# Kernel optimization log

Measured on AMD Instinct MI355X. Metric: run time of the kernel, lower is better.

Reference implementation:

```python
import jax, jax.numpy as jnp
import numpy as np

B, S, D_MODEL, H, D_HEAD = 1, 4096, 512, 8, 64
ROPE_BASE = 10000.0


def setup_inputs() -> dict:
    key = jax.random.key(0)
    ks = jax.random.split(key, 5)
    return {
        "hidden_states": jax.random.normal(ks[0], (B, S, D_MODEL), dtype=jnp.float32),
        "mask": jnp.zeros((B, H, S, S), dtype=jnp.float32),  # additive mask (0 = attend)
        "position_ids": jnp.broadcast_to(jnp.arange(S, dtype=jnp.int64), (B, S)),
        "Wq": jax.random.normal(ks[1], (D_MODEL, H * D_HEAD), dtype=jnp.float32) * 0.02,
        "Wk": jax.random.normal(ks[2], (D_MODEL, H * D_HEAD), dtype=jnp.float32) * 0.02,
        "Wv": jax.random.normal(ks[3], (D_MODEL, H * D_HEAD), dtype=jnp.float32) * 0.02,
        "Wo": jax.random.normal(ks[4], (H * D_HEAD, D_MODEL), dtype=jnp.float32) * 0.02,
    }


def _rope_cos_sin(position_ids, dtype):
    # inv_freq: [D_HEAD//2]
    inv_freq = 1.0 / (ROPE_BASE ** (jnp.arange(0, D_HEAD, 2, dtype=jnp.float32) / D_HEAD))
    freqs = position_ids.astype(jnp.float32)[:, :, None] * inv_freq[None, None, :]  # [b,s,d/2]
    emb = jnp.concatenate([freqs, freqs], axis=-1)  # [b,s,d]
    return jnp.cos(emb).astype(dtype), jnp.sin(emb).astype(dtype)


def _rotate_half(x):
    x1, x2 = x[..., : D_HEAD // 2], x[..., D_HEAD // 2 :]
    return jnp.concatenate([-x2, x1], axis=-1)


def reference(hidden_states, mask, position_ids, Wq, Wk, Wv, Wo):
    b, s, _ = hidden_states.shape
    shape = lambda x: x.reshape(b, s, H, D_HEAD).transpose(0, 2, 1, 3)  # b h s d
    q = shape(hidden_states @ Wq)
    k = shape(hidden_states @ Wk)
    v = shape(hidden_states @ Wv)

    cos, sin = _rope_cos_sin(position_ids, hidden_states.dtype)
    cos, sin = cos[:, None], sin[:, None]  # broadcast over heads
    q = q * cos + _rotate_half(q) * sin
    k = k * cos + _rotate_half(k) * sin

    # eager attention: NO 1/sqrt(d) scaling, matches the torch module
    scores = jnp.einsum("bhqd,bhkd->bhqk", q, k) + mask
    attn = jax.nn.softmax(scores.astype(jnp.float32), axis=-1).astype(scores.dtype)
    out = jnp.einsum("bhqk,bhkd->bhqd", attn, v)  # b h s d
    out = out.transpose(0, 2, 1, 3).reshape(b, s, H * D_HEAD)
    return out @ Wo
```

## Files before the change

### kernel.cpp

```cpp
#include <hip/hip_runtime.h>
#include <hip/hip_bf16.h>

typedef short s16x8 __attribute__((ext_vector_type(8)));
typedef float f32x4 __attribute__((ext_vector_type(4)));
typedef float f32x16 __attribute__((ext_vector_type(16)));

#define SQ 4096
#define DMODEL 512
#define NHEAD 8
#define DHEAD 64
#define LOG2E 1.4426950408889634f

static __device__ __forceinline__ unsigned short f2bf(float f) {
  unsigned int u = __float_as_uint(f);
  u += 0x7FFFu + ((u >> 16) & 1u);
  return (unsigned short)(u >> 16);
}

static __device__ __forceinline__ f32x4 MFMA16(s16x8 a, s16x8 b, f32x4 c) {
  return __builtin_amdgcn_mfma_f32_16x16x32_bf16(a, b, c, 0, 0, 0);
}
static __device__ __forceinline__ f32x16 MFMA32(s16x8 a, s16x8 b, f32x16 c) {
  return __builtin_amdgcn_mfma_f32_32x32x16_bf16(a, b, c, 0, 0, 0);
}
static __device__ __forceinline__ unsigned int cvtpk(float lo, float hi) {
  unsigned int r;
  asm("v_cvt_pk_bf16_f32 %0, %1, %2" : "=v"(r) : "v"(lo), "v"(hi));
  return r;
}
static __device__ __forceinline__ void plswap(unsigned int& x, unsigned int& y) {
  asm("v_permlane32_swap_b32 %0, %1" : "+v"(x), "+v"(y));
}
static __device__ __forceinline__ void gload_lds16(const unsigned short* g, unsigned short* l) {
  __builtin_amdgcn_global_load_lds((const __attribute__((address_space(1))) void*)g,
                                   (__attribute__((address_space(3))) void*)l, 16, 0, 0);
}

__global__ void rope_table_kernel(float* __restrict__ cos_t, float* __restrict__ sin_t) {
  int idx = blockIdx.x * 256 + threadIdx.x;
  int s = idx >> 5, i = idx & 31;
  float inv = exp2f(-(float)i * 0.4152410118609203f);
  float th = (float)s * inv;
  float sv, cv;
  sincosf(th, &sv, &cv);
  cos_t[idx] = cv;
  sin_t[idx] = sv;
}

__global__ __launch_bounds__(256) void qkv_kernel(
    const float* __restrict__ X, const float* __restrict__ Wq,
    const float* __restrict__ Wk, const float* __restrict__ Wv,
    const float* __restrict__ cos_t, const float* __restrict__ sin_t,
    unsigned short* __restrict__ Qf, unsigned short* __restrict__ Kf,
    unsigned short* __restrict__ Vf) {
  __shared__ __align__(16) unsigned short WT[64][40];
  __shared__ __align__(16) unsigned short Ts[64][72];
  const int pz = blockIdx.z;
  const float* __restrict__ W = (pz == 0) ? Wq : ((pz == 1) ? Wk : Wv);
  unsigned short* __restrict__ Out = (pz == 0) ? Qf : ((pz == 1) ? Kf : Vf);
  const int rb = blockIdx.x * 64;
  const int h  = blockIdx.y;
  const int cb = h * 64;
  const int t = threadIdx.x;
  const int w = t >> 6, l = t & 63;
  const int c = l & 15, g = l >> 4;

  f32x4 acc[4];
#pragma unroll
  for (int n = 0; n < 4; n++) acc[n] = (f32x4){0.f, 0.f, 0.f, 0.f};

  const int a2 = t >> 4;
  const int cm = (t & 15) * 4;
  const float* __restrict__ xp0 = X + (size_t)(rb + w * 16 + c) * DMODEL + g * 8;

  for (int kb = 0; kb < DMODEL; kb += 32) {
    {
      const float* wp = W + (size_t)(kb + 2 * a2) * DMODEL + cb + cm;
      float4 w0 = *(const float4*)wp;
      float4 w1 = *(const float4*)(wp + DMODEL);
      unsigned int p0 = (unsigned int)f2bf(w0.x) | ((unsigned int)f2bf(w1.x) << 16);
      unsigned int p1 = (unsigned int)f2bf(w0.y) | ((unsigned int)f2bf(w1.y) << 16);
      unsigned int p2 = (unsigned int)f2bf(w0.z) | ((unsigned int)f2bf(w1.z) << 16);
      unsigned int p3 = (unsigned int)f2bf(w0.w) | ((unsigned int)f2bf(w1.w) << 16);
      *(unsigned int*)&WT[cm + 0][2 * a2] = p0;
      *(unsigned int*)&WT[cm + 1][2 * a2] = p1;
      *(unsigned int*)&WT[cm + 2][2 * a2] = p2;
      *(unsigned int*)&WT[cm + 3][2 * a2] = p3;
    }
    __syncthreads();
    float4 x0 = *(const float4*)(xp0 + kb);
    float4 x1 = *(const float4*)(xp0 + kb + 4);
    s16x8 af;
    af[0] = (short)f2bf(x0.x); af[1] = (short)f2bf(x0.y);
    af[2] = (short)f2bf(x0.z); af[3] = (short)f2bf(x0.w);
    af[4] = (short)f2bf(x1.x); af[5] = (short)f2bf(x1.y);
    af[6] = (short)f2bf(x1.z); af[7] = (short)f2bf(x1.w);
#pragma unroll
    for (int n = 0; n < 4; n++) {
      s16x8 bf = *(const s16x8*)&WT[n * 16 + c][g * 8];
      acc[n] = MFMA16(af, bf, acc[n]);
    }
    __syncthreads();
  }

  if (pz < 2) {
    const float qs = (pz == 0) ? LOG2E : 1.0f;
#pragma unroll
    for (int n = 0; n < 2; n++)
#pragma unroll
      for (int i = 0; i < 4; i++) {
        int d = n * 16 + c;
        int sl = w * 16 + g * 4 + i;
        int s = rb + sl;
        float x1v = acc[n][i], x2v = acc[n + 2][i];
        float cv = cos_t[s * 32 + d];
        float sv = sin_t[s * 32 + d];
        Ts[sl][d]      = f2bf((x1v * cv - x2v * sv) * qs);
        Ts[sl][d + 32] = f2bf((x2v * cv + x1v * sv) * qs);
      }
    __syncthreads();
#pragma unroll
    for (int e = 0; e < 2; e++) {
      int f = t * 2 + e;
      int kg = f >> 8, m = (f >> 6) & 3, hif = (f >> 5) & 1, k32 = f & 31;
      s16x8 vv = *(const s16x8*)&Ts[kg * 32 + k32][m * 16 + hif * 8];
      size_t o16 = ((((size_t)h * 128 + (rb >> 5) + kg) * 4 + m) * 2 + hif) * 32 + k32;
      *(s16x8*)(Out + o16 * 8) = vv;
    }
  } else {
#pragma unroll
    for (int n = 0; n < 4; n++) {
      int d = n * 16 + c;
      int s0 = w * 16 + g * 4;
      unsigned int lo = (unsigned int)f2bf(acc[n][0]) | ((unsigned int)f2bf(acc[n][1]) << 16);
      unsigned int hi2 = (unsigned int)f2bf(acc[n][2]) | ((unsigned int)f2bf(acc[n][3]) << 16);
      *(unsigned int*)&Ts[d][s0]     = lo;
      *(unsigned int*)&Ts[d][s0 + 2] = hi2;
    }
    __syncthreads();
#pragma unroll
    for (int e = 0; e < 2; e++) {
      int f = t * 2 + e;
      int ktr = f >> 7, dc = (f >> 6) & 1, hif = (f >> 5) & 1, d32 = f & 31;
      s16x8 vv = *(const s16x8*)&Ts[dc * 32 + d32][ktr * 16 + hif * 8];
      size_t o16 = ((((size_t)h * 256 + (rb >> 4) + ktr) * 2 + dc) * 2 + hif) * 32 + d32;
      *(s16x8*)(Out + o16 * 8) = vv;
    }
  }
}

__global__ __launch_bounds__(256, 2) void attn_kernel(
    const unsigned short* __restrict__ Qf, const unsigned short* __restrict__ Kf,
    const unsigned short* __restrict__ Vf, float* __restrict__ Opart,
    float* __restrict__ Ml) {
  __shared__ __align__(16) unsigned short Sl[8192];
  const int h = blockIdx.y, part = blockIdx.z;
  const int qb = blockIdx.x * 128;
  const int t = threadIdx.x, w = t >> 6, l = t & 63;
  const int l31 = l & 31, hi = l >> 5;

  s16x8 qf[4];
  {
    const unsigned short* qp =
        Qf + ((((size_t)h * 128 + ((qb + w * 32) >> 5)) * 4) * 64 + l) * 8;
#pragma unroll
    for (int m = 0; m < 4; m++) qf[m] = *(const s16x8*)(qp + (size_t)m * 512);
  }
  f32x16 oacc0 = {}, oacc1 = {};
  float mi = -1e30f, li = 0.f;

  const unsigned short* Kit = Kf + ((size_t)h * 128 + part * 64) * 2048;
  const unsigned short* Vit = Vf + ((size_t)h * 256 + part * 128) * 1024;

  for (int it = 0; it < 32; ++it) {
    __syncthreads();
    {
      const unsigned short* src =
          (w < 2) ? (Kit + (size_t)it * 4096 + (size_t)w * 2048 + l * 8)
                  : (Vit + (size_t)it * 4096 + (size_t)(w - 2) * 2048 + l * 8);
      unsigned short* dst = Sl + w * 2048 + l * 8;
#pragma unroll
      for (int j = 0; j < 4; j++) gload_lds16(src + j * 512, dst + j * 512);
    }
    __syncthreads();

#pragma unroll
    for (int kgl = 0; kgl < 2; ++kgl) {
      s16x8 kf0 = *(const s16x8*)&Sl[kgl * 2048 + 0 * 512 + l * 8];
      s16x8 kf1 = *(const s16x8*)&Sl[kgl * 2048 + 1 * 512 + l * 8];
      s16x8 kf2 = *(const s16x8*)&Sl[kgl * 2048 + 2 * 512 + l * 8];
      s16x8 kf3 = *(const s16x8*)&Sl[kgl * 2048 + 3 * 512 + l * 8];
      f32x16 st = {};
      __builtin_amdgcn_s_setprio(1);
      st = MFMA32(kf0, qf[0], st);
      st = MFMA32(kf1, qf[1], st);
      st = MFMA32(kf2, qf[2], st);
      st = MFMA32(kf3, qf[3], st);
      __builtin_amdgcn_s_setprio(0);

      float tmax = st[0];
#pragma unroll
      for (int r = 1; r < 16; ++r) tmax = fmaxf(tmax, st[r]);
      tmax = fmaxf(tmax, __shfl_xor(tmax, 32));
      if (!__all(tmax <= mi + 8.0f)) {
        float mn = fmaxf(mi, tmax);
        float al = exp2f(mi - mn);
        mi = mn;
        li *= al;
#pragma unroll
        for (int r = 0; r < 16; ++r) {
          int qv = (r & 3) + 8 * (r >> 2) + 4 * hi;
          float aq = __shfl(al, qv);
          oacc0[r] *= aq;
          oacc1[r] *= aq;
        }
      }
      float p[16];
      float rs = 0.f;
#pragma unroll
      for (int r = 0; r < 16; ++r) {
        p[r] = exp2f(st[r] - mi);
        rs += p[r];
      }
      rs += __shfl_xor(rs, 32);
      li += rs;

      unsigned int u0 = cvtpk(p[0], p[1]),   u1 = cvtpk(p[2], p[3]);
      unsigned int u2 = cvtpk(p[4], p[5]),   u3 = cvtpk(p[6], p[7]);
      unsigned int u4 = cvtpk(p[8], p[9]),   u5 = cvtpk(p[10], p[11]);
      unsigned int u6 = cvtpk(p[12], p[13]), u7 = cvtpk(p[14], p[15]);
      plswap(u0, u2);
      plswap(u1, u3);
      plswap(u4, u6);
      plswap(u5, u7);
      union { unsigned int u[4]; s16x8 v; } P0, P1;
      P0.u[0] = u0; P0.u[1] = u1; P0.u[2] = u2; P0.u[3] = u3;
      P1.u[0] = u4; P1.u[1] = u5; P1.u[2] = u6; P1.u[3] = u7;

      s16x8 vf00 = *(const s16x8*)&Sl[4096 + (kgl * 2 + 0) * 1024 + 0 * 512 + l * 8];
      s16x8 vf01 = *(const s16x8*)&Sl[4096 + (kgl * 2 + 0) * 1024 + 1 * 512 + l * 8];
      s16x8 vf10 = *(const s16x8*)&Sl[4096 + (kgl * 2 + 1) * 1024 + 0 * 512 + l * 8];
      s16x8 vf11 = *(const s16x8*)&Sl[4096 + (kgl * 2 + 1) * 1024 + 1 * 512 + l * 8];
      __builtin_amdgcn_s_setprio(1);
      oacc0 = MFMA32(P0.v, vf00, oacc0);
      oacc1 = MFMA32(P0.v, vf01, oacc1);
      oacc0 = MFMA32(P1.v, vf10, oacc0);
      oacc1 = MFMA32(P1.v, vf11, oacc1);
      __builtin_amdgcn_s_setprio(0);
    }
  }

  float* Ob = Opart + (((size_t)(part * 8 + h) * 4096) + qb + w * 32) * 64;
#pragma unroll
  for (int r = 0; r < 16; ++r) {
    int qv = (r & 3) + 8 * (r >> 2) + 4 * hi;
    Ob[(size_t)qv * 64 + l31]      = oacc0[r];
    Ob[(size_t)qv * 64 + 32 + l31] = oacc1[r];
  }
  if (hi == 0) {
    float2 mlv = make_float2(mi, li);
    *(float2*)&Ml[((size_t)(part * 8 + h) * 4096 + qb + w * 32 + l31) * 2] = mlv;
  }
}

__global__ __launch_bounds__(256) void merge_kernel(
    const float* __restrict__ Opart, const float* __restrict__ Ml,
    unsigned short* __restrict__ AO) {
  int tid = blockIdx.x * 256 + threadIdx.x;
  int q = tid >> 9, hd = tid & 511, h = hd >> 6, d = hd & 63;
  size_t b1 = (size_t)h * 4096 + q;
  size_t b2 = (size_t)(8 + h) * 4096 + q;
  float m1 = Ml[b1 * 2], l1 = Ml[b1 * 2 + 1];
  float m2 = Ml[b2 * 2], l2 = Ml[b2 * 2 + 1];
  float mm = fmaxf(m1, m2);
  float w1 = exp2f(m1 - mm), w2 = exp2f(m2 - mm);
  float o = Opart[b1 * 64 + d] * w1 + Opart[b2 * 64 + d] * w2;
  AO[tid] = f2bf(o / (l1 * w1 + l2 * w2));
}

__global__ __launch_bounds__(256) void oproj_kernel(
    const unsigned short* __restrict__ A, const float* __restrict__ Wo,
    float* __restrict__ Out) {
  __shared__ __align__(16) unsigned short WT[64][40];
  const int rb = blockIdx.x * 64;
  const int cb = blockIdx.y * 64;
  const int t = threadIdx.x;
  const int w = t >> 6, l = t & 63;
  const int c = l & 15, g = l >> 4;

  f32x4 acc[4];
#pragma unroll
  for (int n = 0; n < 4; n++) acc[n] = (f32x4){0.f, 0.f, 0.f, 0.f};

  const int a2 = t >> 4, cm = (t & 15) * 4;
  const unsigned short* __restrict__ ap0 = A + (size_t)(rb + w * 16 + c) * DMODEL + g * 8;

  for (int kb = 0; kb < DMODEL; kb += 32) {
    {
      const float* wp = Wo + (size_t)(kb + 2 * a2) * DMODEL + cb + cm;
      float4 w0 = *(const float4*)wp;
      float4 w1 = *(const float4*)(wp + DMODEL);
      unsigned int p0 = (unsigned int)f2bf(w0.x) | ((unsigned int)f2bf(w1.x) << 16);
      unsigned int p1 = (unsigned int)f2bf(w0.y) | ((unsigned int)f2bf(w1.y) << 16);
      unsigned int p2 = (unsigned int)f2bf(w0.z) | ((unsigned int)f2bf(w1.z) << 16);
      unsigned int p3 = (unsigned int)f2bf(w0.w) | ((unsigned int)f2bf(w1.w) << 16);
      *(unsigned int*)&WT[cm + 0][2 * a2] = p0;
      *(unsigned int*)&WT[cm + 1][2 * a2] = p1;
      *(unsigned int*)&WT[cm + 2][2 * a2] = p2;
      *(unsigned int*)&WT[cm + 3][2 * a2] = p3;
    }
    __syncthreads();
    s16x8 af = *(const s16x8*)(ap0 + kb);
#pragma unroll
    for (int n = 0; n < 4; n++) {
      s16x8 bf = *(const s16x8*)&WT[n * 16 + c][g * 8];
      acc[n] = MFMA16(af, bf, acc[n]);
    }
    __syncthreads();
  }

#pragma unroll
  for (int n = 0; n < 4; n++)
#pragma unroll
    for (int i = 0; i < 4; i++) {
      int s = rb + w * 16 + g * 4 + i;
      Out[(size_t)s * DMODEL + cb + n * 16 + c] = acc[n][i];
    }
}

extern "C" void kernel_launch(void* const* d_in, const int* in_sizes, int n_in,
                              void* d_out, int out_size, void* d_ws, size_t ws_size,
                              hipStream_t stream) {
  const float* X  = (const float*)d_in[0];
  const float* Wq = (const float*)d_in[3];
  const float* Wk = (const float*)d_in[4];
  const float* Wv = (const float*)d_in[5];
  const float* Wo = (const float*)d_in[6];
  float* out = (float*)d_out;

  char* ws = (char*)d_ws;
  const size_t HSZ = (size_t)NHEAD * SQ * DHEAD;
  unsigned short* Qf = (unsigned short*)ws;
  unsigned short* Kf = Qf + HSZ;
  unsigned short* Vf = Kf + HSZ;
  unsigned short* AO = Vf + HSZ;
  float* Opart = (float*)(ws + 4 * HSZ * sizeof(unsigned short));
  float* Ml    = Opart + 2 * HSZ;
  float* cos_t = Ml + (size_t)2 * NHEAD * SQ * 2;
  float* sin_t = cos_t + (size_t)SQ * 32;

  rope_table_kernel<<<(SQ * 32) / 256, 256, 0, stream>>>(cos_t, sin_t);
  qkv_kernel<<<dim3(SQ / 64, NHEAD, 3), 256, 0, stream>>>(
      X, Wq, Wk, Wv, cos_t, sin_t, Qf, Kf, Vf);
  attn_kernel<<<dim3(SQ / 128, NHEAD, 2), 256, 0, stream>>>(Qf, Kf, Vf, Opart, Ml);
  merge_kernel<<<(int)(HSZ / 256), 256, 0, stream>>>(Opart, Ml, AO);
  oproj_kernel<<<dim3(SQ / 64, DMODEL / 64), 256, 0, stream>>>(AO, Wo, out);
}
```

Before: 132.9 us.

## Pre-convert weights to bf16, double-buffer LDS, fuse merge into oproj

A prep kernel now converts all four weight matrices to bf16 once, alongside building the RoPE table, so the GEMM kernels no longer convert fp32 weights in every tile. The qkv and oproj kernels double-buffer their weight tiles in LDS and prefetch the next k-slice into registers, which removes one barrier per iteration. The attention kernel double-buffers its K/V LDS stages so the next tile's global-to-LDS load overlaps compute. The split-KV merge is folded into oproj's A-operand load, removing a kernel launch and the AO round trip at the cost of more LDS and more registers.

```diff
diff --git a/kernel.cpp b/kernel.cpp
--- a/kernel.cpp
+++ b/kernel.cpp
@@ -1,6 +1,7 @@
 #include <hip/hip_runtime.h>
 #include <hip/hip_bf16.h>
 
+typedef short s16x4 __attribute__((ext_vector_type(4)));
 typedef short s16x8 __attribute__((ext_vector_type(8)));
 typedef float f32x4 __attribute__((ext_vector_type(4)));
 typedef float f32x16 __attribute__((ext_vector_type(16)));
@@ -36,27 +37,42 @@
                                    (__attribute__((address_space(3))) void*)l, 16, 0, 0);
 }
 
-__global__ void rope_table_kernel(float* __restrict__ cos_t, float* __restrict__ sin_t) {
-  int idx = blockIdx.x * 256 + threadIdx.x;
-  int s = idx >> 5, i = idx & 31;
-  float inv = exp2f(-(float)i * 0.4152410118609203f);
-  float th = (float)s * inv;
-  float sv, cv;
-  sincosf(th, &sv, &cv);
-  cos_t[idx] = cv;
-  sin_t[idx] = sv;
+__global__ void prep_kernel(const float* __restrict__ Wq, const float* __restrict__ Wk,
+                            const float* __restrict__ Wv, const float* __restrict__ Wo,
+                            float* __restrict__ cos_t, float* __restrict__ sin_t,
+                            unsigned short* __restrict__ WB) {
+  int b = blockIdx.x;
+  if (b < 512) {
+    int idx = b * 256 + threadIdx.x;
+    int s = idx >> 5, i = idx & 31;
+    float inv = exp2f(-(float)i * 0.4152410118609203f);
+    float th = (float)s * inv;
+    float sv, cv;
+    sincosf(th, &sv, &cv);
+    cos_t[idx] = cv;
+    sin_t[idx] = sv;
+  } else {
+    int bb = b - 512;
+    int mat = bb >> 8;
+    const float* __restrict__ W = (mat == 0) ? Wq : (mat == 1) ? Wk : (mat == 2) ? Wv : Wo;
+    int e = ((bb & 255) * 256 + threadIdx.x) * 4;
+    float4 v = *(const float4*)(W + e);
+    s16x4 o;
+    o[0] = (short)f2bf(v.x); o[1] = (short)f2bf(v.y);
+    o[2] = (short)f2bf(v.z); o[3] = (short)f2bf(v.w);
+    *(s16x4*)(WB + (size_t)mat * 262144 + e) = o;
+  }
 }
 
 __global__ __launch_bounds__(256) void qkv_kernel(
-    const float* __restrict__ X, const float* __restrict__ Wq,
-    const float* __restrict__ Wk, const float* __restrict__ Wv,
+    const float* __restrict__ X, const unsigned short* __restrict__ WB,
     const float* __restrict__ cos_t, const float* __restrict__ sin_t,
     unsigned short* __restrict__ Qf, unsigned short* __restrict__ Kf,
     unsigned short* __restrict__ Vf) {
-  __shared__ __align__(16) unsigned short WT[64][40];
+  __shared__ __align__(16) unsigned short WT[2][64][36];
   __shared__ __align__(16) unsigned short Ts[64][72];
   const int pz = blockIdx.z;
-  const float* __restrict__ W = (pz == 0) ? Wq : ((pz == 1) ? Wk : Wv);
+  const unsigned short* __restrict__ W = WB + (size_t)pz * 262144;
   unsigned short* __restrict__ Out = (pz == 0) ? Qf : ((pz == 1) ? Kf : Vf);
   const int rb = blockIdx.x * 64;
   const int h  = blockIdx.y;
@@ -65,40 +81,52 @@
   const int w = t >> 6, l = t & 63;
   const int c = l & 15, g = l >> 4;
 
-  f32x4 acc[4];
-#pragma unroll
-  for (int n = 0; n < 4; n++) acc[n] = (f32x4){0.f, 0.f, 0.f, 0.f};
-
+  f32x4 acc[4] = {};
   const int a2 = t >> 4;
   const int cm = (t & 15) * 4;
   const float* __restrict__ xp0 = X + (size_t)(rb + w * 16 + c) * DMODEL + g * 8;
-
-  for (int kb = 0; kb < DMODEL; kb += 32) {
-    {
-      const float* wp = W + (size_t)(kb + 2 * a2) * DMODEL + cb + cm;
-      float4 w0 = *(const float4*)wp;
-      float4 w1 = *(const float4*)(wp + DMODEL);
-      unsigned int p0 = (unsigned int)f2bf(w0.x) | ((unsigned int)f2bf(w1.x) << 16);
-      unsigned int p1 = (unsigned int)f2bf(w0.y) | ((unsigned int)f2bf(w1.y) << 16);
-      unsigned int p2 = (unsigned int)f2bf(w0.z) | ((unsigned int)f2bf(w1.z) << 16);
-      unsigned int p3 = (unsigned int)f2bf(w0.w) | ((unsigned int)f2bf(w1.w) << 16);
-      *(unsigned int*)&WT[cm + 0][2 * a2] = p0;
-      *(unsigned int*)&WT[cm + 1][2 * a2] = p1;
-      *(unsigned int*)&WT[cm + 2][2 * a2] = p2;
-      *(unsigned int*)&WT[cm + 3][2 * a2] = p3;
-    }
-    __syncthreads();
-    float4 x0 = *(const float4*)(xp0 + kb);
-    float4 x1 = *(const float4*)(xp0 + kb + 4);
+  const unsigned short* __restrict__ wp0 = W + (size_t)(2 * a2) * DMODEL + cb + cm;
+
+  {
+    s16x4 w0 = *(const s16x4*)wp0;
+    s16x4 w1 = *(const s16x4*)(wp0 + DMODEL);
+#pragma unroll
+    for (int j = 0; j < 4; j++)
+      *(unsigned int*)&WT[0][cm + j][2 * a2] =
+          (unsigned int)(unsigned short)w0[j] | ((unsigned int)(unsigned short)w1[j] << 16);
+  }
+  float4 xc0 = *(const float4*)xp0;
+  float4 xc1 = *(const float4*)(xp0 + 4);
+  __syncthreads();
+
+  for (int i = 0; i < 16; ++i) {
+    const int cur = i & 1;
+    s16x4 nw0, nw1;
+    float4 xn0, xn1;
+    if (i < 15) {
+      const unsigned short* wp = wp0 + (size_t)(i + 1) * 32 * DMODEL;
+      nw0 = *(const s16x4*)wp;
+      nw1 = *(const s16x4*)(wp + DMODEL);
+      xn0 = *(const float4*)(xp0 + (i + 1) * 32);
+      xn1 = *(const float4*)(xp0 + (i + 1) * 32 + 4);
+    }
     s16x8 af;
-    af[0] = (short)f2bf(x0.x); af[1] = (short)f2bf(x0.y);
-    af[2] = (short)f2bf(x0.z); af[3] = (short)f2bf(x0.w);
-    af[4] = (short)f2bf(x1.x); af[5] = (short)f2bf(x1.y);
-    af[6] = (short)f2bf(x1.z); af[7] = (short)f2bf(x1.w);
+    af[0] = (short)f2bf(xc0.x); af[1] = (short)f2bf(xc0.y);
+    af[2] = (short)f2bf(xc0.z); af[3] = (short)f2bf(xc0.w);
+    af[4] = (short)f2bf(xc1.x); af[5] = (short)f2bf(xc1.y);
+    af[6] = (short)f2bf(xc1.z); af[7] = (short)f2bf(xc1.w);
 #pragma unroll
     for (int n = 0; n < 4; n++) {
-      s16x8 bf = *(const s16x8*)&WT[n * 16 + c][g * 8];
+      s16x8 bf = *(const s16x8*)&WT[cur][n * 16 + c][g * 8];
       acc[n] = MFMA16(af, bf, acc[n]);
+    }
+    if (i < 15) {
+#pragma unroll
+      for (int j = 0; j < 4; j++)
+        *(unsigned int*)&WT[cur ^ 1][cm + j][2 * a2] =
+            (unsigned int)(unsigned short)nw0[j] | ((unsigned int)(unsigned short)nw1[j] << 16);
+      xc0 = xn0;
+      xc1 = xn1;
     }
     __syncthreads();
   }
@@ -153,7 +181,7 @@
     const unsigned short* __restrict__ Qf, const unsigned short* __restrict__ Kf,
     const unsigned short* __restrict__ Vf, float* __restrict__ Opart,
     float* __restrict__ Ml) {
-  __shared__ __align__(16) unsigned short Sl[8192];
+  __shared__ __align__(16) unsigned short Sl[2][8192];
   const int h = blockIdx.y, part = blockIdx.z;
   const int qb = blockIdx.x * 128;
   const int t = threadIdx.x, w = t >> 6, l = t & 63;
@@ -172,24 +200,34 @@
   const unsigned short* Kit = Kf + ((size_t)h * 128 + part * 64) * 2048;
   const unsigned short* Vit = Vf + ((size_t)h * 256 + part * 128) * 1024;
 
+#define STAGE(buf, it)                                                                  \
+  {                                                                                     \
+    const unsigned short* src =                                                         \
+        (w < 2) ? (Kit + (size_t)(it) * 4096 + (size_t)w * 2048 + l * 8)                \
+                : (Vit + (size_t)(it) * 4096 + (size_t)(w - 2) * 2048 + l * 8);         \
+    unsigned short* dst = &Sl[buf][w * 2048 + l * 8];                                   \
+    gload_lds16(src + 0 * 512, dst + 0 * 512);                                          \
+    gload_lds16(src + 1 * 512, dst + 1 * 512);                                          \
+    gload_lds16(src + 2 * 512, dst + 2 * 512);                                          \
+    gload_lds16(src + 3 * 512, dst + 3 * 512);                                          \
+  }
+
+  STAGE(0, 0);
+  asm volatile("s_waitcnt vmcnt(0)" ::: "memory");
+  __builtin_amdgcn_s_barrier();
+  asm volatile("" ::: "memory");
+
   for (int it = 0; it < 32; ++it) {
-    __syncthreads();
-    {
-      const unsigned short* src =
-          (w < 2) ? (Kit + (size_t)it * 4096 + (size_t)w * 2048 + l * 8)
-                  : (Vit + (size_t)it * 4096 + (size_t)(w - 2) * 2048 + l * 8);
-      unsigned short* dst = Sl + w * 2048 + l * 8;
-#pragma unroll
-      for (int j = 0; j < 4; j++) gload_lds16(src + j * 512, dst + j * 512);
-    }
-    __syncthreads();
+    const int cur = it & 1;
+    if (it < 31) STAGE(cur ^ 1, it + 1);
+    const unsigned short* Sb = &Sl[cur][0];
 
 #pragma unroll
     for (int kgl = 0; kgl < 2; ++kgl) {
-      s16x8 kf0 = *(const s16x8*)&Sl[kgl * 2048 + 0 * 512 + l * 8];
-      s16x8 kf1 = *(const s16x8*)&Sl[kgl * 2048 + 1 * 512 + l * 8];
-      s16x8 kf2 = *(const s16x8*)&Sl[kgl * 2048 + 2 * 512 + l * 8];
-      s16x8 kf3 = *(const s16x8*)&Sl[kgl * 2048 + 3 * 512 + l * 8];
+      s16x8 kf0 = *(const s16x8*)&Sb[kgl * 2048 + 0 * 512 + l * 8];
+      s16x8 kf1 = *(const s16x8*)&Sb[kgl * 2048 + 1 * 512 + l * 8];
+      s16x8 kf2 = *(const s16x8*)&Sb[kgl * 2048 + 2 * 512 + l * 8];
+      s16x8 kf3 = *(const s16x8*)&Sb[kgl * 2048 + 3 * 512 + l * 8];
       f32x16 st = {};
       __builtin_amdgcn_s_setprio(1);
       st = MFMA32(kf0, qf[0], st);
@@ -237,10 +275,10 @@
       P0.u[0] = u0; P0.u[1] = u1; P0.u[2] = u2; P0.u[3] = u3;
       P1.u[0] = u4; P1.u[1] = u5; P1.u[2] = u6; P1.u[3] = u7;
 
-      s16x8 vf00 = *(const s16x8*)&Sl[4096 + (kgl * 2 + 0) * 1024 + 0 * 512 + l * 8];
-      s16x8 vf01 = *(const s16x8*)&Sl[4096 + (kgl * 2 + 0) * 1024 + 1 * 512 + l * 8];
-      s16x8 vf10 = *(const s16x8*)&Sl[4096 + (kgl * 2 + 1) * 1024 + 0 * 512 + l * 8];
-      s16x8 vf11 = *(const s16x8*)&Sl[4096 + (kgl * 2 + 1) * 1024 + 1 * 512 + l * 8];
+      s16x8 vf00 = *(const s16x8*)&Sb[4096 + (kgl * 2 + 0) * 1024 + 0 * 512 + l * 8];
+      s16x8 vf01 = *(const s16x8*)&Sb[4096 + (kgl * 2 + 0) * 1024 + 1 * 512 + l * 8];
+      s16x8 vf10 = *(const s16x8*)&Sb[4096 + (kgl * 2 + 1) * 1024 + 0 * 512 + l * 8];
+      s16x8 vf11 = *(const s16x8*)&Sb[4096 + (kgl * 2 + 1) * 1024 + 1 * 512 + l * 8];
       __builtin_amdgcn_s_setprio(1);
       oacc0 = MFMA32(P0.v, vf00, oacc0);
       oacc1 = MFMA32(P0.v, vf01, oacc1);
@@ -248,7 +286,12 @@
       oacc1 = MFMA32(P1.v, vf11, oacc1);
       __builtin_amdgcn_s_setprio(0);
     }
-  }
+
+    asm volatile("s_waitcnt vmcnt(0)" ::: "memory");
+    __builtin_amdgcn_s_barrier();
+    asm volatile("" ::: "memory");
+  }
+#undef STAGE
 
   float* Ob = Opart + (((size_t)(part * 8 + h) * 4096) + qb + w * 32) * 64;
 #pragma unroll
@@ -263,68 +306,93 @@
   }
 }
 
-__global__ __launch_bounds__(256) void merge_kernel(
+__global__ __launch_bounds__(256) void oproj_kernel(
     const float* __restrict__ Opart, const float* __restrict__ Ml,
-    unsigned short* __restrict__ AO) {
-  int tid = blockIdx.x * 256 + threadIdx.x;
-  int q = tid >> 9, hd = tid & 511, h = hd >> 6, d = hd & 63;
-  size_t b1 = (size_t)h * 4096 + q;
-  size_t b2 = (size_t)(8 + h) * 4096 + q;
-  float m1 = Ml[b1 * 2], l1 = Ml[b1 * 2 + 1];
-  float m2 = Ml[b2 * 2], l2 = Ml[b2 * 2 + 1];
-  float mm = fmaxf(m1, m2);
-  float w1 = exp2f(m1 - mm), w2 = exp2f(m2 - mm);
-  float o = Opart[b1 * 64 + d] * w1 + Opart[b2 * 64 + d] * w2;
-  AO[tid] = f2bf(o / (l1 * w1 + l2 * w2));
-}
-
-__global__ __launch_bounds__(256) void oproj_kernel(
-    const unsigned short* __restrict__ A, const float* __restrict__ Wo,
-    float* __restrict__ Out) {
-  __shared__ __align__(16) unsigned short WT[64][40];
+    const unsigned short* __restrict__ WoB, float* __restrict__ Out) {
+  __shared__ __align__(16) unsigned short WT[2][64][36];
   const int rb = blockIdx.x * 64;
   const int cb = blockIdx.y * 64;
   const int t = threadIdx.x;
   const int w = t >> 6, l = t & 63;
   const int c = l & 15, g = l >> 4;
 
-  f32x4 acc[4];
-#pragma unroll
-  for (int n = 0; n < 4; n++) acc[n] = (f32x4){0.f, 0.f, 0.f, 0.f};
-
+  f32x4 acc[4] = {};
   const int a2 = t >> 4, cm = (t & 15) * 4;
-  const unsigned short* __restrict__ ap0 = A + (size_t)(rb + w * 16 + c) * DMODEL + g * 8;
-
-  for (int kb = 0; kb < DMODEL; kb += 32) {
-    {
-      const float* wp = Wo + (size_t)(kb + 2 * a2) * DMODEL + cb + cm;
-      float4 w0 = *(const float4*)wp;
-      float4 w1 = *(const float4*)(wp + DMODEL);
-      unsigned int p0 = (unsigned int)f2bf(w0.x) | ((unsigned int)f2bf(w1.x) << 16);
-      unsigned int p1 = (unsigned int)f2bf(w0.y) | ((unsigned int)f2bf(w1.y) << 16);
-      unsigned int p2 = (unsigned int)f2bf(w0.z) | ((unsigned int)f2bf(w1.z) << 16);
-      unsigned int p3 = (unsigned int)f2bf(w0.w) | ((unsigned int)f2bf(w1.w) << 16);
-      *(unsigned int*)&WT[cm + 0][2 * a2] = p0;
-      *(unsigned int*)&WT[cm + 1][2 * a2] = p1;
-      *(unsigned int*)&WT[cm + 2][2 * a2] = p2;
-      *(unsigned int*)&WT[cm + 3][2 * a2] = p3;
+  const int s = rb + w * 16 + c;
+
+  float a1[8], a2w[8];
+#pragma unroll
+  for (int hh = 0; hh < 8; hh++) {
+    float2 ml1 = *(const float2*)&Ml[((size_t)hh * 4096 + s) * 2];
+    float2 ml2 = *(const float2*)&Ml[((size_t)(8 + hh) * 4096 + s) * 2];
+    float mm = fmaxf(ml1.x, ml2.x);
+    float w1 = exp2f(ml1.x - mm), w2 = exp2f(ml2.x - mm);
+    float invL = 1.0f / (ml1.y * w1 + ml2.y * w2);
+    a1[hh] = w1 * invL;
+    a2w[hh] = w2 * invL;
+  }
+
+  const unsigned short* __restrict__ wp0 = WoB + (size_t)(2 * a2) * DMODEL + cb + cm;
+  {
+    s16x4 w0 = *(const s16x4*)wp0;
+    s16x4 w1 = *(const s16x4*)(wp0 + DMODEL);
+#pragma unroll
+    for (int j = 0; j < 4; j++)
+      *(unsigned int*)&WT[0][cm + j][2 * a2] =
+          (unsigned int)(unsigned short)w0[j] | ((unsigned int)(unsigned short)w1[j] << 16);
+  }
+  const float* op1b = Opart + (size_t)s * 64 + g * 8;
+  const float* op2b = op1b + (size_t)8 * 4096 * 64;
+  float4 pa0 = *(const float4*)op1b, pa1 = *(const float4*)(op1b + 4);
+  float4 pb0 = *(const float4*)op2b, pb1 = *(const float4*)(op2b + 4);
+  __syncthreads();
+
+#pragma unroll
+  for (int i = 0; i < 16; ++i) {
+    const int cur = i & 1;
+    const int hh = i >> 1;
+    s16x4 nw0, nw1;
+    float4 na0, na1, nb0, nb1;
+    if (i < 15) {
+      const unsigned short* wp = wp0 + (size_t)(i + 1) * 32 * DMODEL;
+      nw0 = *(const s16x4*)wp;
+      nw1 = *(const s16x4*)(wp + DMODEL);
+      size_t ao = (size_t)(i + 1 >> 1) * 4096 * 64 + ((i + 1) & 1) * 32;
+      na0 = *(const float4*)(op1b + ao);
+      na1 = *(const float4*)(op1b + ao + 4);
+      nb0 = *(const float4*)(op2b + ao);
+      nb1 = *(const float4*)(op2b + ao + 4);
+    }
+    s16x8 af;
+    af[0] = (short)f2bf(pa0.x * a1[hh] + pb0.x * a2w[hh]);
+    af[1] = (short)f2bf(pa0.y * a1[hh] + pb0.y * a2w[hh]);
+    af[2] = (short)f2bf(pa0.z * a1[hh] + pb0.z * a2w[hh]);
+    af[3] = (short)f2bf(pa0.w * a1[hh] + pb0.w * a2w[hh]);
+    af[4] = (short)f2bf(pa1.x * a1[hh] + pb1.x * a2w[hh]);
+    af[5] = (short)f2bf(pa1.y * a1[hh] + pb1.y * a2w[hh]);
+    af[6] = (short)f2bf(pa1.z * a1[hh] + pb1.z * a2w[hh]);
+    af[7] = (short)f2bf(pa1.w * a1[hh] + pb1.w * a2w[hh]);
+#pragma unroll
+    for (int n = 0; n < 4; n++) {
+      s16x8 bf = *(const s16x8*)&WT[cur][n * 16 + c][g * 8];
+      acc[n] = MFMA16(af, bf, acc[n]);
+    }
+    if (i < 15) {
+#pragma unroll
+      for (int j = 0; j < 4; j++)
+        *(unsigned int*)&WT[cur ^ 1][cm + j][2 * a2] =
+            (unsigned int)(unsigned short)nw0[j] | ((unsigned int)(unsigned short)nw1[j] << 16);
+      pa0 = na0; pa1 = na1; pb0 = nb0; pb1 = nb1;
     }
     __syncthreads();
-    s16x8 af = *(const s16x8*)(ap0 + kb);
-#pragma unroll
-    for (int n = 0; n < 4; n++) {
-      s16x8 bf = *(const s16x8*)&WT[n * 16 + c][g * 8];
-      acc[n] = MFMA16(af, bf, acc[n]);
-    }
-    __syncthreads();
   }
 
 #pragma unroll
   for (int n = 0; n < 4; n++)
 #pragma unroll
     for (int i = 0; i < 4; i++) {
-      int s = rb + w * 16 + g * 4 + i;
-      Out[(size_t)s * DMODEL + cb + n * 16 + c] = acc[n][i];
+      int s2 = rb + w * 16 + g * 4 + i;
+      Out[(size_t)s2 * DMODEL + cb + n * 16 + c] = acc[n][i];
     }
 }
 
@@ -343,16 +411,16 @@
   unsigned short* Qf = (unsigned short*)ws;
   unsigned short* Kf = Qf + HSZ;
   unsigned short* Vf = Kf + HSZ;
-  unsigned short* AO = Vf + HSZ;
-  float* Opart = (float*)(ws + 4 * HSZ * sizeof(unsigned short));
+  float* Opart = (float*)(ws + 3 * HSZ * sizeof(unsigned short));
   float* Ml    = Opart + 2 * HSZ;
-  float* cos_t = Ml + (size_t)2 * NHEAD * SQ * 2;
+  float* cos_t = Ml + 131072;
   float* sin_t = cos_t + (size_t)SQ * 32;
-
-  rope_table_kernel<<<(SQ * 32) / 256, 256, 0, stream>>>(cos_t, sin_t);
+  unsigned short* WB = (unsigned short*)(sin_t + (size_t)SQ * 32);
+
+  prep_kernel<<<1536, 256, 0, stream>>>(Wq, Wk, Wv, Wo, cos_t, sin_t, WB);
   qkv_kernel<<<dim3(SQ / 64, NHEAD, 3), 256, 0, stream>>>(
-      X, Wq, Wk, Wv, cos_t, sin_t, Qf, Kf, Vf);
+      X, WB, cos_t, sin_t, Qf, Kf, Vf);
   attn_kernel<<<dim3(SQ / 128, NHEAD, 2), 256, 0, stream>>>(Qf, Kf, Vf, Opart, Ml);
-  merge_kernel<<<(int)(HSZ / 256), 256, 0, stream>>>(Opart, Ml, AO);
-  oproj_kernel<<<dim3(SQ / 64, DMODEL / 64), 256, 0, stream>>>(AO, Wo, out);
-}
+  oproj_kernel<<<dim3(SQ / 64, DMODEL / 64), 256, 0, stream>>>(
+      Opart, Ml, WB + (size_t)3 * 262144, out);
+}
```

Result: faster. 125.9 us (-5.3%).
